# Performance work log

Hardware: AMD Instinct MI355X
Metric: run time of the kernel (lower is better)

The kernel has to match this reference:

```python
import jax, jax.numpy as jnp
import numpy as np

B, DIN, DOUT, DC, K, DB = 4096, 512, 512, 64, 16, 256
NEG = 0.01
LN_EPS = 1e-5

def _lrelu(v):
    return jnp.where(v >= 0, v, NEG * v)

def setup_inputs() -> dict:
    key = jax.random.key(0)
    ks = jax.random.split(key, 12)
    bound = 1.0 / np.sqrt(DIN)
    def u(k, shape, b):
        return jax.random.uniform(k, shape, jnp.float32, -b, b)
    return {
        "x": jax.random.normal(ks[0], (B, DIN), jnp.float32),
        "c": jax.random.normal(ks[1], (B, DC), jnp.float32),
        "ln_gamma": jnp.ones((DIN,), jnp.float32),
        "ln_beta": jnp.zeros((DIN,), jnp.float32),
        "w1": u(ks[2], (DC, DB), 1.0 / np.sqrt(DC)),
        "b1": u(ks[3], (DB,), 1.0 / np.sqrt(DC)),
        "wr": u(ks[4], (DB, DB), 1.0 / np.sqrt(DB)),
        "br": u(ks[5], (DB,), 1.0 / np.sqrt(DB)),
        "w2": u(ks[6], (DB, K), 1.0 / np.sqrt(DB)),
        "b2": u(ks[7], (K,), 1.0 / np.sqrt(DB)),
        "W": u(ks[8], (K, DIN, DOUT), bound),
        "bvec": u(ks[9], (K, DOUT), bound),
    }

def reference(x, c, ln_gamma, ln_beta, w1, b1, wr, br, w2, b2, W, bvec):
    # DenseActivation: LayerNorm + LeakyReLU (dropout_rate=0)
    mu = jnp.mean(x, axis=-1, keepdims=True)
    var = jnp.mean(jnp.square(x - mu), axis=-1, keepdims=True)
    xn = (x - mu) * jax.lax.rsqrt(var + LN_EPS) * ln_gamma + ln_beta
    a = _lrelu(xn)  # [B, DIN]
    # basis_functions(c): Linear -> 1 preactivation resnet block -> LeakyReLU -> Linear
    h = c @ w1 + b1                      # [B, DB]
    h = h + (_lrelu(h) @ wr + br)        # residual block (preactivation)
    h = _lrelu(h)                        # activate_output
    bf = h @ w2 + b2                     # [B, K]
    # out_b = x_b^T (sum_k bf_bk W_k) + bf_b @ bias ; reordered contraction
    xw = jnp.einsum("bi,kio->bko", a, W)       # [B, K, DOUT]
    out = jnp.einsum("bk,bko->bo", bf, xw)     # [B, DOUT]
    out = out + bf @ bvec
    return out
```

## Files before the change

### kernel.cpp

```cpp
#include <hip/hip_runtime.h>


#define LRELU(v) ((v) >= 0.f ? (v) : 0.01f * (v))

typedef _Float16 f16x8 __attribute__((ext_vector_type(8)));
typedef float f32x4 __attribute__((ext_vector_type(4)));

#define GL16(gp, lp) __builtin_amdgcn_global_load_lds(                      \
    (const __attribute__((address_space(1))) void*)(gp),                    \
    (__attribute__((address_space(3))) void*)(lp), 16, 0, 0)

#define MFMA16(a, b, c) __builtin_amdgcn_mfma_f32_16x16x32_f16((a), (b), (c), 0, 0, 0)

__global__ __launch_bounds__(256) void prep_kernel(
    const float* __restrict__ x, const float* __restrict__ gam,
    const float* __restrict__ bet, _Float16* __restrict__ a,
    const float* __restrict__ c, const float* __restrict__ w1,
    const float* __restrict__ b1, const float* __restrict__ wr,
    const float* __restrict__ br, const float* __restrict__ w2,
    const float* __restrict__ b2, float* __restrict__ bfo,
    const float* __restrict__ W, _Float16* __restrict__ Wt)
{
    __shared__ __align__(16) char smem[18432];
    int tid = threadIdx.x;
    int blk = blockIdx.x;

    if (blk < 512) {
        float* c_l  = (float*)smem;
        float* lr_l = (float*)(smem + 2048);
        float* h_l  = (float*)(smem + 10240);
        int b0 = blk * 8;

        for (int i = tid; i < 8 * 64; i += 256) c_l[i] = c[(size_t)b0 * 64 + i];

        float w1c[64];
#pragma unroll
        for (int u = 0; u < 64; ++u) w1c[u] = w1[u * 256 + tid];
        float b1s = b1[tid];
        __syncthreads();

        float h1[8];
#pragma unroll
        for (int r = 0; r < 8; ++r) h1[r] = b1s;
#pragma unroll
        for (int j4 = 0; j4 < 16; ++j4) {
#pragma unroll
            for (int r = 0; r < 8; ++r) {
                float4 cv = *(const float4*)&c_l[r * 64 + j4 * 4];
                h1[r] += cv.x * w1c[j4 * 4 + 0] + cv.y * w1c[j4 * 4 + 1] +
                         cv.z * w1c[j4 * 4 + 2] + cv.w * w1c[j4 * 4 + 3];
            }
        }
#pragma unroll
        for (int r = 0; r < 8; ++r) lr_l[r * 256 + tid] = LRELU(h1[r]);
        __syncthreads();

        float brv = br[tid];
        float h2[8];
#pragma unroll
        for (int r = 0; r < 8; ++r) h2[r] = h1[r] + brv;

#pragma unroll 1
        for (int jc = 0; jc < 8; ++jc) {
            float w8[32];
#pragma unroll
            for (int u = 0; u < 32; ++u) w8[u] = wr[(jc * 32 + u) * 256 + tid];
#pragma unroll
            for (int j4 = 0; j4 < 8; ++j4) {
#pragma unroll
                for (int r = 0; r < 8; ++r) {
                    float4 lv = *(const float4*)&lr_l[r * 256 + jc * 32 + j4 * 4];
                    h2[r] += lv.x * w8[j4 * 4 + 0] + lv.y * w8[j4 * 4 + 1] +
                             lv.z * w8[j4 * 4 + 2] + lv.w * w8[j4 * 4 + 3];
                }
            }
        }
#pragma unroll
        for (int r = 0; r < 8; ++r) h_l[r * 256 + tid] = LRELU(h2[r]);
        __syncthreads();

        if (tid < 128) {
            int r = tid >> 4, k = tid & 15;
            float s = b2[k];
#pragma unroll 1
            for (int qc = 0; qc < 8; ++qc) {
                float wv[32];
#pragma unroll
                for (int u = 0; u < 32; ++u) wv[u] = w2[(qc * 32 + u) * 16 + k];
#pragma unroll
                for (int q4 = 0; q4 < 8; ++q4) {
                    float4 hv = *(const float4*)&h_l[r * 256 + qc * 32 + q4 * 4];
                    s += hv.x * wv[q4 * 4 + 0] + hv.y * wv[q4 * 4 + 1] +
                         hv.z * wv[q4 * 4 + 2] + hv.w * wv[q4 * 4 + 3];
                }
            }
            bfo[(size_t)(b0 + r) * 16 + k] = s;
        }

    } else if (blk < 1536) {
        float* t = (float*)smem;
        int bid = blk - 512;
        int k  = bid >> 6;
        int it = (bid >> 3) & 7;
        int ot = bid & 7;
        int i0 = it * 64, o0 = ot * 64;

        int rr = tid >> 4, c4 = (tid & 15) * 4;
#pragma unroll
        for (int p = 0; p < 4; ++p) {
            int r = p * 16 + rr;
            float4 v = *(const float4*)&W[((size_t)(k * 512 + i0 + r)) * 512 + o0 + c4];
            t[r * 65 + c4 + 0] = v.x;
            t[r * 65 + c4 + 1] = v.y;
            t[r * 65 + c4 + 2] = v.z;
            t[r * 65 + c4 + 3] = v.w;
        }
        __syncthreads();

        int ol = tid >> 2, c0 = (tid & 3) * 16;
        _Float16 hb[16] __attribute__((aligned(16)));
#pragma unroll
        for (int u = 0; u < 16; ++u) hb[u] = (_Float16)t[(c0 + u) * 65 + ol];
        _Float16* dst = &Wt[(size_t)(o0 + ol) * 8192 + k * 512 + i0 + c0];
        *(float4*)dst       = *(const float4*)&hb[0];
        *(float4*)(dst + 8) = *(const float4*)&hb[8];

    } else {
        int lane = tid & 63;
        int row  = (blk - 1536) * 4 + (tid >> 6);
        const float* xr = x + (size_t)row * 512 + lane * 8;
        float4 v0 = *(const float4*)xr;
        float4 v1 = *(const float4*)(xr + 4);

        float s = v0.x + v0.y + v0.z + v0.w + v1.x + v1.y + v1.z + v1.w;
#pragma unroll
        for (int m = 1; m < 64; m <<= 1) s += __shfl_xor(s, m);
        float mean = s * (1.f / 512.f);

        float d, s2 = 0.f;
        d = v0.x - mean; s2 += d * d;
        d = v0.y - mean; s2 += d * d;
        d = v0.z - mean; s2 += d * d;
        d = v0.w - mean; s2 += d * d;
        d = v1.x - mean; s2 += d * d;
        d = v1.y - mean; s2 += d * d;
        d = v1.z - mean; s2 += d * d;
        d = v1.w - mean; s2 += d * d;
#pragma unroll
        for (int m = 1; m < 64; m <<= 1) s2 += __shfl_xor(s2, m);
        float rstd = rsqrtf(s2 * (1.f / 512.f) + 1e-5f);

        float4 g0 = *(const float4*)&gam[lane * 8];
        float4 g1 = *(const float4*)&gam[lane * 8 + 4];
        float4 b0 = *(const float4*)&bet[lane * 8];
        float4 b1v = *(const float4*)&bet[lane * 8 + 4];

        _Float16 o8[8] __attribute__((aligned(16)));
        float y;
        y = (v0.x - mean) * rstd * g0.x + b0.x;  y = LRELU(y); o8[0] = (_Float16)y;
        y = (v0.y - mean) * rstd * g0.y + b0.y;  y = LRELU(y); o8[1] = (_Float16)y;
        y = (v0.z - mean) * rstd * g0.z + b0.z;  y = LRELU(y); o8[2] = (_Float16)y;
        y = (v0.w - mean) * rstd * g0.w + b0.w;  y = LRELU(y); o8[3] = (_Float16)y;
        y = (v1.x - mean) * rstd * g1.x + b1v.x; y = LRELU(y); o8[4] = (_Float16)y;
        y = (v1.y - mean) * rstd * g1.y + b1v.y; y = LRELU(y); o8[5] = (_Float16)y;
        y = (v1.z - mean) * rstd * g1.z + b1v.z; y = LRELU(y); o8[6] = (_Float16)y;
        y = (v1.w - mean) * rstd * g1.w + b1v.w; y = LRELU(y); o8[7] = (_Float16)y;

        *(float4*)&a[(size_t)row * 512 + lane * 8] = *(const float4*)o8;
    }
}

template <int NSPLIT>
__global__ __launch_bounds__(256, 2) void gemm_kernel(
    const _Float16* __restrict__ A,
    const _Float16* __restrict__ Wt,
    const float* __restrict__ bfg,
    const float* __restrict__ bvec,
    _Float16* __restrict__ pout)
{
    constexpr int KTN = 16 / NSPLIT;
    constexpr int NT  = KTN * 8;

    __shared__ _Float16 As[2][128 * 64];
    __shared__ _Float16 Bs[2][128 * 64];

    const int tid = threadIdx.x;
    const int bid = blockIdx.x;
    const int split = bid % NSPLIT;
    const int mn  = bid / NSPLIT;
    const int n0  = (mn & 3) * 128;
    const int bm0 = (mn >> 2) * 128;
    const int kt0 = split * KTN;

    const int lane = tid & 63, wid = tid >> 6;
    const int wm = wid >> 1, wn = wid & 1;
    const int l16 = lane & 15, lg = lane >> 4;

    _Float16 s16[KTN][4];
#pragma unroll
    for (int kt = 0; kt < KTN; ++kt)
#pragma unroll
        for (int f = 0; f < 4; ++f)
            s16[kt][f] = (_Float16)
                bfg[(size_t)(bm0 + wm * 64 + f * 16 + l16) * 16 + kt0 + kt];

    const int brow = tid >> 3;
    const int swc  = (tid & 7) ^ (brow & 7);
    const _Float16* aAs = A  + (size_t)(bm0 + brow) * 512  + swc * 8;
    const _Float16* aBs = Wt + (size_t)(n0  + brow) * 8192 + swc * 8;

    auto STAGE = [&](int t, int buf) {
        const int ka = (t & 7) * 64;
        const size_t kb = (size_t)(kt0 + (t >> 3)) * 512 + ka;
        char* la = (char*)&As[buf][0] + tid * 16;
        char* lb = (char*)&Bs[buf][0] + tid * 16;
#pragma unroll
        for (int p = 0; p < 4; ++p) {
            GL16(aAs + (size_t)(p * 32) * 512 + ka, la + p * 4096);
            GL16(aBs + (size_t)(p * 32) * 8192 + kb, lb + p * 4096);
        }
    };

    const int swr = l16 & 7;
    const int aRowByte = (wm * 64 + l16) * 128;
    const int bRowByte = (wn * 64 + l16) * 128;
    const int sw0 = ((0 + lg) ^ swr) << 4;
    const int sw1 = ((4 + lg) ^ swr) << 4;

    const f32x4 z4 = {0.f, 0.f, 0.f, 0.f};
    f32x4 acc[4][4];
#pragma unroll
    for (int f = 0; f < 4; ++f)
#pragma unroll
        for (int nf = 0; nf < 4; ++nf) acc[f][nf] = z4;

    STAGE(0, 0);
    STAGE(1, 1);
    asm volatile("s_waitcnt vmcnt(8)" ::: "memory");
    __builtin_amdgcn_s_barrier();
    __builtin_amdgcn_sched_barrier(0);

#pragma unroll
    for (int kt = 0; kt < KTN; ++kt) {
#pragma unroll 1
        for (int t2 = 0; t2 < 8; ++t2) {
            const int t = kt * 8 + t2;
            const int cur = t & 1;
            const char* Ab = (const char*)&As[cur][0];
            const char* Bb = (const char*)&Bs[cur][0];
            const int tt = t + 2;
            const bool st = (tt < NT);
            char* sAd = (char*)&As[cur][0] + tid * 16;
            char* sBd = (char*)&Bs[cur][0] + tid * 16;
            const int ka = (tt & 7) * 64;
            const size_t kb = (size_t)(kt0 + (tt >> 3)) * 512 + ka;

            f16x8 bA0 = *(const f16x8*)(Bb + bRowByte + 0 * 2048 + sw0);
            f16x8 bA1 = *(const f16x8*)(Bb + bRowByte + 0 * 2048 + sw1);
            f16x8 bB0 = *(const f16x8*)(Bb + bRowByte + 1 * 2048 + sw0);
            f16x8 bB1 = *(const f16x8*)(Bb + bRowByte + 1 * 2048 + sw1);
            f16x8 bC0 = *(const f16x8*)(Bb + bRowByte + 2 * 2048 + sw0);
            f16x8 bC1 = *(const f16x8*)(Bb + bRowByte + 2 * 2048 + sw1);
            f16x8 bD0 = *(const f16x8*)(Bb + bRowByte + 3 * 2048 + sw0);
            f16x8 bD1 = *(const f16x8*)(Bb + bRowByte + 3 * 2048 + sw1);
            f16x8 a00 = *(const f16x8*)(Ab + aRowByte + 0 * 2048 + sw0);
            f16x8 a01 = *(const f16x8*)(Ab + aRowByte + 0 * 2048 + sw1);
            f16x8 a10 = *(const f16x8*)(Ab + aRowByte + 1 * 2048 + sw0);
            f16x8 a11 = *(const f16x8*)(Ab + aRowByte + 1 * 2048 + sw1);
            __builtin_amdgcn_s_barrier();

            {
                const _Float16 s0 = s16[kt][0], s1 = s16[kt][1];
                a00 *= s0; a01 *= s0; a10 *= s1; a11 *= s1;
                __builtin_amdgcn_s_setprio(1);
                acc[0][0] = MFMA16(a00, bA0, acc[0][0]);
                acc[0][0] = MFMA16(a01, bA1, acc[0][0]);
                acc[0][1] = MFMA16(a00, bB0, acc[0][1]);
                acc[0][1] = MFMA16(a01, bB1, acc[0][1]);
                acc[0][2] = MFMA16(a00, bC0, acc[0][2]);
                acc[0][2] = MFMA16(a01, bC1, acc[0][2]);
                acc[0][3] = MFMA16(a00, bD0, acc[0][3]);
                acc[0][3] = MFMA16(a01, bD1, acc[0][3]);
                acc[1][0] = MFMA16(a10, bA0, acc[1][0]);
                acc[1][0] = MFMA16(a11, bA1, acc[1][0]);
                acc[1][1] = MFMA16(a10, bB0, acc[1][1]);
                acc[1][1] = MFMA16(a11, bB1, acc[1][1]);
                acc[1][2] = MFMA16(a10, bC0, acc[1][2]);
                acc[1][2] = MFMA16(a11, bC1, acc[1][2]);
                acc[1][3] = MFMA16(a10, bD0, acc[1][3]);
                acc[1][3] = MFMA16(a11, bD1, acc[1][3]);
                __builtin_amdgcn_s_setprio(0);
            }
            __builtin_amdgcn_s_barrier();

            f16x8 a20 = *(const f16x8*)(Ab + aRowByte + 2 * 2048 + sw0);
            f16x8 a21 = *(const f16x8*)(Ab + aRowByte + 2 * 2048 + sw1);
            f16x8 a30 = *(const f16x8*)(Ab + aRowByte + 3 * 2048 + sw0);
            f16x8 a31 = *(const f16x8*)(Ab + aRowByte + 3 * 2048 + sw1);
            if (st) {
                GL16(aBs + (size_t)(0 * 32) * 8192 + kb, sBd + 0 * 4096);
                GL16(aBs + (size_t)(1 * 32) * 8192 + kb, sBd + 1 * 4096);
                GL16(aBs + (size_t)(2 * 32) * 8192 + kb, sBd + 2 * 4096);
                GL16(aBs + (size_t)(3 * 32) * 8192 + kb, sBd + 3 * 4096);
                GL16(aAs + (size_t)(0 * 32) * 512 + ka, sAd + 0 * 4096);
                GL16(aAs + (size_t)(2 * 32) * 512 + ka, sAd + 2 * 4096);
            }
            __builtin_amdgcn_s_barrier();

            {
                const _Float16 s2 = s16[kt][2], s3 = s16[kt][3];
                a20 *= s2; a21 *= s2; a30 *= s3; a31 *= s3;
                __builtin_amdgcn_s_setprio(1);
                acc[2][0] = MFMA16(a20, bA0, acc[2][0]);
                acc[2][0] = MFMA16(a21, bA1, acc[2][0]);
                acc[2][1] = MFMA16(a20, bB0, acc[2][1]);
                acc[2][1] = MFMA16(a21, bB1, acc[2][1]);
                acc[2][2] = MFMA16(a20, bC0, acc[2][2]);
                acc[2][2] = MFMA16(a21, bC1, acc[2][2]);
                acc[2][3] = MFMA16(a20, bD0, acc[2][3]);
                acc[2][3] = MFMA16(a21, bD1, acc[2][3]);
                acc[3][0] = MFMA16(a30, bA0, acc[3][0]);
                acc[3][0] = MFMA16(a31, bA1, acc[3][0]);
                acc[3][1] = MFMA16(a30, bB0, acc[3][1]);
                acc[3][1] = MFMA16(a31, bB1, acc[3][1]);
                acc[3][2] = MFMA16(a30, bC0, acc[3][2]);
                acc[3][2] = MFMA16(a31, bC1, acc[3][2]);
                acc[3][3] = MFMA16(a30, bD0, acc[3][3]);
                acc[3][3] = MFMA16(a31, bD1, acc[3][3]);
                __builtin_amdgcn_s_setprio(0);
            }
            __builtin_amdgcn_s_barrier();

            if (st) {
                GL16(aAs + (size_t)(1 * 32) * 512 + ka, sAd + 1 * 4096);
                GL16(aAs + (size_t)(3 * 32) * 512 + ka, sAd + 3 * 4096);
                asm volatile("s_waitcnt vmcnt(8)" ::: "memory");
            } else {
                asm volatile("s_waitcnt vmcnt(0)" ::: "memory");
            }
            __builtin_amdgcn_s_barrier();
            __builtin_amdgcn_sched_barrier(0);
        }
    }

    _Float16* op = pout + (size_t)split * (4096 * 512);
    const int colBase = n0 + wn * 64 + l16;
    float bvv[KTN][4];
#pragma unroll
    for (int kt = 0; kt < KTN; ++kt)
#pragma unroll
        for (int nf = 0; nf < 4; ++nf)
            bvv[kt][nf] = bvec[(kt0 + kt) * 512 + colBase + nf * 16];

#pragma unroll
    for (int f = 0; f < 4; ++f)
#pragma unroll
        for (int j = 0; j < 4; ++j) {
            const int grow = bm0 + wm * 64 + f * 16 + lg * 4 + j;
            const float* bfr = &bfg[(size_t)grow * 16 + kt0];
            float bfl[KTN];
#pragma unroll
            for (int kt = 0; kt < KTN; ++kt) bfl[kt] = bfr[kt];
            _Float16* orow = op + (size_t)grow * 512 + colBase;
#pragma unroll
            for (int nf = 0; nf < 4; ++nf) {
                float v = acc[f][nf][j];
#pragma unroll
                for (int kt = 0; kt < KTN; ++kt) v += bfl[kt] * bvv[kt][nf];
                orow[nf * 16] = (_Float16)v;
            }
        }
}

__global__ __launch_bounds__(256) void reduce_kernel(const _Float16* __restrict__ p,
                                                     float* __restrict__ out,
                                                     int nsplit)
{
    size_t i   = (size_t)blockIdx.x * 256 + threadIdx.x;
    size_t off = i * 8;
    float s[8] = {0.f, 0.f, 0.f, 0.f, 0.f, 0.f, 0.f, 0.f};
    for (int sp = 0; sp < nsplit; ++sp) {
        f16x8 v = *(const f16x8*)&p[(size_t)sp * 2097152 + off];
#pragma unroll
        for (int u = 0; u < 8; ++u) s[u] += (float)v[u];
    }
    float4 o0 = {s[0], s[1], s[2], s[3]};
    float4 o1 = {s[4], s[5], s[6], s[7]};
    *(float4*)&out[off]     = o0;
    *(float4*)&out[off + 4] = o1;
}

extern "C" void kernel_launch(void* const* d_in, const int* in_sizes, int n_in,
                              void* d_out, int out_size, void* d_ws, size_t ws_size,
                              hipStream_t stream)
{
    const float* x    = (const float*)d_in[0];
    const float* c    = (const float*)d_in[1];
    const float* gam  = (const float*)d_in[2];
    const float* bet  = (const float*)d_in[3];
    const float* w1   = (const float*)d_in[4];
    const float* b1   = (const float*)d_in[5];
    const float* wr   = (const float*)d_in[6];
    const float* br   = (const float*)d_in[7];
    const float* w2   = (const float*)d_in[8];
    const float* b2   = (const float*)d_in[9];
    const float* W    = (const float*)d_in[10];
    const float* bvec = (const float*)d_in[11];
    float* out = (float*)d_out;

    const int nsplit = 4;
    const size_t partBytes = (size_t)nsplit * 4096 * 512 * sizeof(_Float16);

    char* ws = (char*)d_ws;
    _Float16* part = (_Float16*)ws;
    _Float16* Wt   = (_Float16*)(ws + partBytes);
    _Float16* af   = (_Float16*)(ws + partBytes + (8u << 20));
    float*    bf   = (float*)(ws + partBytes + (12u << 20));

    prep_kernel<<<dim3(2560), dim3(256), 0, stream>>>(
        x, gam, bet, af, c, w1, b1, wr, br, w2, b2, bf, W, Wt);

    gemm_kernel<4><<<dim3(512), dim3(256), 0, stream>>>(af, Wt, bf, bvec, part);

    reduce_kernel<<<dim3(1024), dim3(256), 0, stream>>>(part, out, nsplit);
}
```

Before: 82.89 us.

## Replace double-buffered GEMM pipeline with single-buffer, more splits and higher occupancy

```diff
diff --git a/kernel.cpp b/kernel.cpp
--- a/kernel.cpp
+++ b/kernel.cpp
@@ -171,7 +171,7 @@
 }
 
 template <int NSPLIT>
-__global__ __launch_bounds__(256, 2) void gemm_kernel(
+__global__ __launch_bounds__(256, 4) void gemm_kernel(
     const _Float16* __restrict__ A,
     const _Float16* __restrict__ Wt,
     const float* __restrict__ bfg,
@@ -179,10 +179,9 @@
     _Float16* __restrict__ pout)
 {
     constexpr int KTN = 16 / NSPLIT;
-    constexpr int NT  = KTN * 8;
-
-    __shared__ _Float16 As[2][128 * 64];
-    __shared__ _Float16 Bs[2][128 * 64];
+
+    __shared__ _Float16 As[128 * 64];
+    __shared__ _Float16 Bs[128 * 64];
 
     const int tid = threadIdx.x;
     const int bid = blockIdx.x;
@@ -204,22 +203,12 @@
             s16[kt][f] = (_Float16)
                 bfg[(size_t)(bm0 + wm * 64 + f * 16 + l16) * 16 + kt0 + kt];
 
-    const int brow = tid >> 3;
-    const int swc  = (tid & 7) ^ (brow & 7);
-    const _Float16* aAs = A  + (size_t)(bm0 + brow) * 512  + swc * 8;
-    const _Float16* aBs = Wt + (size_t)(n0  + brow) * 8192 + swc * 8;
-
-    auto STAGE = [&](int t, int buf) {
-        const int ka = (t & 7) * 64;
-        const size_t kb = (size_t)(kt0 + (t >> 3)) * 512 + ka;
-        char* la = (char*)&As[buf][0] + tid * 16;
-        char* lb = (char*)&Bs[buf][0] + tid * 16;
-#pragma unroll
-        for (int p = 0; p < 4; ++p) {
-            GL16(aAs + (size_t)(p * 32) * 512 + ka, la + p * 4096);
-            GL16(aBs + (size_t)(p * 32) * 8192 + kb, lb + p * 4096);
-        }
-    };
+    const int srow = tid >> 3;
+    const int swc  = (tid & 7) ^ (srow & 7);
+    const _Float16* aAs = A  + (size_t)(bm0 + srow) * 512  + swc * 8;
+    const _Float16* aBs = Wt + (size_t)(n0  + srow) * 8192 + swc * 8;
+    char* lA = (char*)As + tid * 16;
+    char* lB = (char*)Bs + tid * 16;
 
     const int swr = l16 & 7;
     const int aRowByte = (wm * 64 + l16) * 128;
@@ -234,26 +223,24 @@
 #pragma unroll
         for (int nf = 0; nf < 4; ++nf) acc[f][nf] = z4;
 
-    STAGE(0, 0);
-    STAGE(1, 1);
-    asm volatile("s_waitcnt vmcnt(8)" ::: "memory");
-    __builtin_amdgcn_s_barrier();
-    __builtin_amdgcn_sched_barrier(0);
+    const char* Ab = (const char*)As;
+    const char* Bb = (const char*)Bs;
 
 #pragma unroll
     for (int kt = 0; kt < KTN; ++kt) {
+        const size_t kcol = (size_t)(kt0 + kt) * 512;
+        const _Float16 s0 = s16[kt][0], s1 = s16[kt][1];
+        const _Float16 s2 = s16[kt][2], s3 = s16[kt][3];
 #pragma unroll 1
-        for (int t2 = 0; t2 < 8; ++t2) {
-            const int t = kt * 8 + t2;
-            const int cur = t & 1;
-            const char* Ab = (const char*)&As[cur][0];
-            const char* Bb = (const char*)&Bs[cur][0];
-            const int tt = t + 2;
-            const bool st = (tt < NT);
-            char* sAd = (char*)&As[cur][0] + tid * 16;
-            char* sBd = (char*)&Bs[cur][0] + tid * 16;
-            const int ka = (tt & 7) * 64;
-            const size_t kb = (size_t)(kt0 + (tt >> 3)) * 512 + ka;
+        for (int ks = 0; ks < 8; ++ks) {
+            const int ka = ks * 64;
+            const size_t kb = kcol + ka;
+#pragma unroll
+            for (int p = 0; p < 4; ++p) {
+                GL16(aAs + (size_t)(p * 32) * 512 + ka, lA + p * 4096);
+                GL16(aBs + (size_t)(p * 32) * 8192 + kb, lB + p * 4096);
+            }
+            __syncthreads();
 
             f16x8 bA0 = *(const f16x8*)(Bb + bRowByte + 0 * 2048 + sw0);
             f16x8 bA1 = *(const f16x8*)(Bb + bRowByte + 0 * 2048 + sw1);
@@ -263,14 +250,12 @@
             f16x8 bC1 = *(const f16x8*)(Bb + bRowByte + 2 * 2048 + sw1);
             f16x8 bD0 = *(const f16x8*)(Bb + bRowByte + 3 * 2048 + sw0);
             f16x8 bD1 = *(const f16x8*)(Bb + bRowByte + 3 * 2048 + sw1);
-            f16x8 a00 = *(const f16x8*)(Ab + aRowByte + 0 * 2048 + sw0);
-            f16x8 a01 = *(const f16x8*)(Ab + aRowByte + 0 * 2048 + sw1);
-            f16x8 a10 = *(const f16x8*)(Ab + aRowByte + 1 * 2048 + sw0);
-            f16x8 a11 = *(const f16x8*)(Ab + aRowByte + 1 * 2048 + sw1);
-            __builtin_amdgcn_s_barrier();
 
             {
-                const _Float16 s0 = s16[kt][0], s1 = s16[kt][1];
+                f16x8 a00 = *(const f16x8*)(Ab + aRowByte + 0 * 2048 + sw0);
+                f16x8 a01 = *(const f16x8*)(Ab + aRowByte + 0 * 2048 + sw1);
+                f16x8 a10 = *(const f16x8*)(Ab + aRowByte + 1 * 2048 + sw0);
+                f16x8 a11 = *(const f16x8*)(Ab + aRowByte + 1 * 2048 + sw1);
                 a00 *= s0; a01 *= s0; a10 *= s1; a11 *= s1;
                 __builtin_amdgcn_s_setprio(1);
                 acc[0][0] = MFMA16(a00, bA0, acc[0][0]);
@@ -291,24 +276,11 @@
                 acc[1][3] = MFMA16(a11, bD1, acc[1][3]);
                 __builtin_amdgcn_s_setprio(0);
             }
-            __builtin_amdgcn_s_barrier();
-
-            f16x8 a20 = *(const f16x8*)(Ab + aRowByte + 2 * 2048 + sw0);
-            f16x8 a21 = *(const f16x8*)(Ab + aRowByte + 2 * 2048 + sw1);
-            f16x8 a30 = *(const f16x8*)(Ab + aRowByte + 3 * 2048 + sw0);
-            f16x8 a31 = *(const f16x8*)(Ab + aRowByte + 3 * 2048 + sw1);
-            if (st) {
-                GL16(aBs + (size_t)(0 * 32) * 8192 + kb, sBd + 0 * 4096);
-                GL16(aBs + (size_t)(1 * 32) * 8192 + kb, sBd + 1 * 4096);
-                GL16(aBs + (size_t)(2 * 32) * 8192 + kb, sBd + 2 * 4096);
-                GL16(aBs + (size_t)(3 * 32) * 8192 + kb, sBd + 3 * 4096);
-                GL16(aAs + (size_t)(0 * 32) * 512 + ka, sAd + 0 * 4096);
-                GL16(aAs + (size_t)(2 * 32) * 512 + ka, sAd + 2 * 4096);
-            }
-            __builtin_amdgcn_s_barrier();
-
             {
-                const _Float16 s2 = s16[kt][2], s3 = s16[kt][3];
+                f16x8 a20 = *(const f16x8*)(Ab + aRowByte + 2 * 2048 + sw0);
+                f16x8 a21 = *(const f16x8*)(Ab + aRowByte + 2 * 2048 + sw1);
+                f16x8 a30 = *(const f16x8*)(Ab + aRowByte + 3 * 2048 + sw0);
+                f16x8 a31 = *(const f16x8*)(Ab + aRowByte + 3 * 2048 + sw1);
                 a20 *= s2; a21 *= s2; a30 *= s3; a31 *= s3;
                 __builtin_amdgcn_s_setprio(1);
                 acc[2][0] = MFMA16(a20, bA0, acc[2][0]);
@@ -329,17 +301,7 @@
                 acc[3][3] = MFMA16(a31, bD1, acc[3][3]);
                 __builtin_amdgcn_s_setprio(0);
             }
-            __builtin_amdgcn_s_barrier();
-
-            if (st) {
-                GL16(aAs + (size_t)(1 * 32) * 512 + ka, sAd + 1 * 4096);
-                GL16(aAs + (size_t)(3 * 32) * 512 + ka, sAd + 3 * 4096);
-                asm volatile("s_waitcnt vmcnt(8)" ::: "memory");
-            } else {
-                asm volatile("s_waitcnt vmcnt(0)" ::: "memory");
-            }
-            __builtin_amdgcn_s_barrier();
-            __builtin_amdgcn_sched_barrier(0);
+            __syncthreads();
         }
     }
 
@@ -408,7 +370,7 @@
     const float* bvec = (const float*)d_in[11];
     float* out = (float*)d_out;
 
-    const int nsplit = 4;
+    const int nsplit = 8;
     const size_t partBytes = (size_t)nsplit * 4096 * 512 * sizeof(_Float16);
 
     char* ws = (char*)d_ws;
@@ -420,7 +382,7 @@
     prep_kernel<<<dim3(2560), dim3(256), 0, stream>>>(
         x, gam, bet, af, c, w1, b1, wr, br, w2, b2, bf, W, Wt);
 
-    gemm_kernel<4><<<dim3(512), dim3(256), 0, stream>>>(af, Wt, bf, bvec, part);
+    gemm_kernel<8><<<dim3(1024), dim3(256), 0, stream>>>(af, Wt, bf, bvec, part);
 
     reduce_kernel<<<dim3(1024), dim3(256), 0, stream>>>(part, out, nsplit);
 }
```

Result: slower. 196.6 us (+137.2%).

## Reorder contraction to GEMM over DIN with in-register k reduction, drop split-K

Applied to the files above, without the earlier changes.

```diff
diff --git a/kernel.cpp b/kernel.cpp
--- a/kernel.cpp
+++ b/kernel.cpp
@@ -19,7 +19,7 @@
     const float* __restrict__ b1, const float* __restrict__ wr,
     const float* __restrict__ br, const float* __restrict__ w2,
     const float* __restrict__ b2, float* __restrict__ bfo,
-    const float* __restrict__ W, _Float16* __restrict__ Wt)
+    const float* __restrict__ W, _Float16* __restrict__ Wp)
 {
     __shared__ __align__(16) char smem[18432];
     int tid = threadIdx.x;
@@ -121,7 +121,7 @@
         _Float16 hb[16] __attribute__((aligned(16)));
 #pragma unroll
         for (int u = 0; u < 16; ++u) hb[u] = (_Float16)t[(c0 + u) * 65 + ol];
-        _Float16* dst = &Wt[(size_t)(o0 + ol) * 8192 + k * 512 + i0 + c0];
+        _Float16* dst = &Wp[((size_t)(o0 + ol) * 16 + k) * 512 + i0 + c0];
         *(float4*)dst       = *(const float4*)&hb[0];
         *(float4*)(dst + 8) = *(const float4*)&hb[8];
 
@@ -170,54 +170,40 @@
     }
 }
 
-template <int NSPLIT>
 __global__ __launch_bounds__(256, 2) void gemm_kernel(
     const _Float16* __restrict__ A,
-    const _Float16* __restrict__ Wt,
+    const _Float16* __restrict__ Wp,
     const float* __restrict__ bfg,
     const float* __restrict__ bvec,
-    _Float16* __restrict__ pout)
+    float* __restrict__ out)
 {
-    constexpr int KTN = 16 / NSPLIT;
-    constexpr int NT  = KTN * 8;
+    constexpr int NT = 8;
 
     __shared__ _Float16 As[2][128 * 64];
     __shared__ _Float16 Bs[2][128 * 64];
 
     const int tid = threadIdx.x;
     const int bid = blockIdx.x;
-    const int split = bid % NSPLIT;
-    const int mn  = bid / NSPLIT;
-    const int n0  = (mn & 3) * 128;
-    const int bm0 = (mn >> 2) * 128;
-    const int kt0 = split * KTN;
+    const int bm0 = (bid >> 6) * 128;
+    const int g0  = (bid & 63) * 128;
 
     const int lane = tid & 63, wid = tid >> 6;
     const int wm = wid >> 1, wn = wid & 1;
     const int l16 = lane & 15, lg = lane >> 4;
 
-    _Float16 s16[KTN][4];
-#pragma unroll
-    for (int kt = 0; kt < KTN; ++kt)
-#pragma unroll
-        for (int f = 0; f < 4; ++f)
-            s16[kt][f] = (_Float16)
-                bfg[(size_t)(bm0 + wm * 64 + f * 16 + l16) * 16 + kt0 + kt];
-
     const int brow = tid >> 3;
     const int swc  = (tid & 7) ^ (brow & 7);
-    const _Float16* aAs = A  + (size_t)(bm0 + brow) * 512  + swc * 8;
-    const _Float16* aBs = Wt + (size_t)(n0  + brow) * 8192 + swc * 8;
+    const _Float16* aAs = A  + (size_t)(bm0 + brow) * 512 + swc * 8;
+    const _Float16* aBs = Wp + (size_t)(g0  + brow) * 512 + swc * 8;
 
     auto STAGE = [&](int t, int buf) {
-        const int ka = (t & 7) * 64;
-        const size_t kb = (size_t)(kt0 + (t >> 3)) * 512 + ka;
+        const int ka = t * 64;
         char* la = (char*)&As[buf][0] + tid * 16;
         char* lb = (char*)&Bs[buf][0] + tid * 16;
 #pragma unroll
         for (int p = 0; p < 4; ++p) {
             GL16(aAs + (size_t)(p * 32) * 512 + ka, la + p * 4096);
-            GL16(aBs + (size_t)(p * 32) * 8192 + kb, lb + p * 4096);
+            GL16(aBs + (size_t)(p * 32) * 512 + ka, lb + p * 4096);
         }
     };
 
@@ -240,154 +226,118 @@
     __builtin_amdgcn_s_barrier();
     __builtin_amdgcn_sched_barrier(0);
 
-#pragma unroll
-    for (int kt = 0; kt < KTN; ++kt) {
 #pragma unroll 1
-        for (int t2 = 0; t2 < 8; ++t2) {
-            const int t = kt * 8 + t2;
-            const int cur = t & 1;
-            const char* Ab = (const char*)&As[cur][0];
-            const char* Bb = (const char*)&Bs[cur][0];
-            const int tt = t + 2;
-            const bool st = (tt < NT);
-            char* sAd = (char*)&As[cur][0] + tid * 16;
-            char* sBd = (char*)&Bs[cur][0] + tid * 16;
-            const int ka = (tt & 7) * 64;
-            const size_t kb = (size_t)(kt0 + (tt >> 3)) * 512 + ka;
-
-            f16x8 bA0 = *(const f16x8*)(Bb + bRowByte + 0 * 2048 + sw0);
-            f16x8 bA1 = *(const f16x8*)(Bb + bRowByte + 0 * 2048 + sw1);
-            f16x8 bB0 = *(const f16x8*)(Bb + bRowByte + 1 * 2048 + sw0);
-            f16x8 bB1 = *(const f16x8*)(Bb + bRowByte + 1 * 2048 + sw1);
-            f16x8 bC0 = *(const f16x8*)(Bb + bRowByte + 2 * 2048 + sw0);
-            f16x8 bC1 = *(const f16x8*)(Bb + bRowByte + 2 * 2048 + sw1);
-            f16x8 bD0 = *(const f16x8*)(Bb + bRowByte + 3 * 2048 + sw0);
-            f16x8 bD1 = *(const f16x8*)(Bb + bRowByte + 3 * 2048 + sw1);
-            f16x8 a00 = *(const f16x8*)(Ab + aRowByte + 0 * 2048 + sw0);
-            f16x8 a01 = *(const f16x8*)(Ab + aRowByte + 0 * 2048 + sw1);
-            f16x8 a10 = *(const f16x8*)(Ab + aRowByte + 1 * 2048 + sw0);
-            f16x8 a11 = *(const f16x8*)(Ab + aRowByte + 1 * 2048 + sw1);
-            __builtin_amdgcn_s_barrier();
-
-            {
-                const _Float16 s0 = s16[kt][0], s1 = s16[kt][1];
-                a00 *= s0; a01 *= s0; a10 *= s1; a11 *= s1;
-                __builtin_amdgcn_s_setprio(1);
-                acc[0][0] = MFMA16(a00, bA0, acc[0][0]);
-                acc[0][0] = MFMA16(a01, bA1, acc[0][0]);
-                acc[0][1] = MFMA16(a00, bB0, acc[0][1]);
-                acc[0][1] = MFMA16(a01, bB1, acc[0][1]);
-                acc[0][2] = MFMA16(a00, bC0, acc[0][2]);
-                acc[0][2] = MFMA16(a01, bC1, acc[0][2]);
-                acc[0][3] = MFMA16(a00, bD0, acc[0][3]);
-                acc[0][3] = MFMA16(a01, bD1, acc[0][3]);
-                acc[1][0] = MFMA16(a10, bA0, acc[1][0]);
-                acc[1][0] = MFMA16(a11, bA1, acc[1][0]);
-                acc[1][1] = MFMA16(a10, bB0, acc[1][1]);
-                acc[1][1] = MFMA16(a11, bB1, acc[1][1]);
-                acc[1][2] = MFMA16(a10, bC0, acc[1][2]);
-                acc[1][2] = MFMA16(a11, bC1, acc[1][2]);
-                acc[1][3] = MFMA16(a10, bD0, acc[1][3]);
-                acc[1][3] = MFMA16(a11, bD1, acc[1][3]);
-                __builtin_amdgcn_s_setprio(0);
+    for (int t = 0; t < NT; ++t) {
+        const int cur = t & 1;
+        const char* Ab = (const char*)&As[cur][0];
+        const char* Bb = (const char*)&Bs[cur][0];
+        const bool st = (t + 2 < NT);
+        char* sAd = (char*)&As[cur][0] + tid * 16;
+        char* sBd = (char*)&Bs[cur][0] + tid * 16;
+        const int ka = (t + 2) * 64;
+
+        f16x8 bA0 = *(const f16x8*)(Bb + bRowByte + 0 * 2048 + sw0);
+        f16x8 bA1 = *(const f16x8*)(Bb + bRowByte + 0 * 2048 + sw1);
+        f16x8 bB0 = *(const f16x8*)(Bb + bRowByte + 1 * 2048 + sw0);
+        f16x8 bB1 = *(const f16x8*)(Bb + bRowByte + 1 * 2048 + sw1);
+        f16x8 bC0 = *(const f16x8*)(Bb + bRowByte + 2 * 2048 + sw0);
+        f16x8 bC1 = *(const f16x8*)(Bb + bRowByte + 2 * 2048 + sw1);
+        f16x8 bD0 = *(const f16x8*)(Bb + bRowByte + 3 * 2048 + sw0);
+        f16x8 bD1 = *(const f16x8*)(Bb + bRowByte + 3 * 2048 + sw1);
+        f16x8 a00 = *(const f16x8*)(Ab + aRowByte + 0 * 2048 + sw0);
+        f16x8 a01 = *(const f16x8*)(Ab + aRowByte + 0 * 2048 + sw1);
+        f16x8 a10 = *(const f16x8*)(Ab + aRowByte + 1 * 2048 + sw0);
+        f16x8 a11 = *(const f16x8*)(Ab + aRowByte + 1 * 2048 + sw1);
+        __builtin_amdgcn_s_barrier();
+
+        __builtin_amdgcn_s_setprio(1);
+        acc[0][0] = MFMA16(a00, bA0, acc[0][0]);
+        acc[0][0] = MFMA16(a01, bA1, acc[0][0]);
+        acc[0][1] = MFMA16(a00, bB0, acc[0][1]);
+        acc[0][1] = MFMA16(a01, bB1, acc[0][1]);
+        acc[0][2] = MFMA16(a00, bC0, acc[0][2]);
+        acc[0][2] = MFMA16(a01, bC1, acc[0][2]);
+        acc[0][3] = MFMA16(a00, bD0, acc[0][3]);
+        acc[0][3] = MFMA16(a01, bD1, acc[0][3]);
+        acc[1][0] = MFMA16(a10, bA0, acc[1][0]);
+        acc[1][0] = MFMA16(a11, bA1, acc[1][0]);
+        acc[1][1] = MFMA16(a10, bB0, acc[1][1]);
+        acc[1][1] = MFMA16(a11, bB1, acc[1][1]);
+        acc[1][2] = MFMA16(a10, bC0, acc[1][2]);
+        acc[1][2] = MFMA16(a11, bC1, acc[1][2]);
+        acc[1][3] = MFMA16(a10, bD0, acc[1][3]);
+        acc[1][3] = MFMA16(a11, bD1, acc[1][3]);
+        __builtin_amdgcn_s_setprio(0);
+        __builtin_amdgcn_s_barrier();
+
+        f16x8 a20 = *(const f16x8*)(Ab + aRowByte + 2 * 2048 + sw0);
+        f16x8 a21 = *(const f16x8*)(Ab + aRowByte + 2 * 2048 + sw1);
+        f16x8 a30 = *(const f16x8*)(Ab + aRowByte + 3 * 2048 + sw0);
+        f16x8 a31 = *(const f16x8*)(Ab + aRowByte + 3 * 2048 + sw1);
+        if (st) {
+            GL16(aBs + (size_t)(0 * 32) * 512 + ka, sBd + 0 * 4096);
+            GL16(aBs + (size_t)(1 * 32) * 512 + ka, sBd + 1 * 4096);
+            GL16(aBs + (size_t)(2 * 32) * 512 + ka, sBd + 2 * 4096);
+            GL16(aBs + (size_t)(3 * 32) * 512 + ka, sBd + 3 * 4096);
+            GL16(aAs + (size_t)(0 * 32) * 512 + ka, sAd + 0 * 4096);
+            GL16(aAs + (size_t)(2 * 32) * 512 + ka, sAd + 2 * 4096);
+        }
+        __builtin_amdgcn_s_barrier();
+
+        __builtin_amdgcn_s_setprio(1);
+        acc[2][0] = MFMA16(a20, bA0, acc[2][0]);
+        acc[2][0] = MFMA16(a21, bA1, acc[2][0]);
+        acc[2][1] = MFMA16(a20, bB0, acc[2][1]);
+        acc[2][1] = MFMA16(a21, bB1, acc[2][1]);
+        acc[2][2] = MFMA16(a20, bC0, acc[2][2]);
+        acc[2][2] = MFMA16(a21, bC1, acc[2][2]);
+        acc[2][3] = MFMA16(a20, bD0, acc[2][3]);
+        acc[2][3] = MFMA16(a21, bD1, acc[2][3]);
+        acc[3][0] = MFMA16(a30, bA0, acc[3][0]);
+        acc[3][0] = MFMA16(a31, bA1, acc[3][0]);
+        acc[3][1] = MFMA16(a30, bB0, acc[3][1]);
+        acc[3][1] = MFMA16(a31, bB1, acc[3][1]);
+        acc[3][2] = MFMA16(a30, bC0, acc[3][2]);
+        acc[3][2] = MFMA16(a31, bC1, acc[3][2]);
+        acc[3][3] = MFMA16(a30, bD0, acc[3][3]);
+        acc[3][3] = MFMA16(a31, bD1, acc[3][3]);
+        __builtin_amdgcn_s_setprio(0);
+        __builtin_amdgcn_s_barrier();
+
+        if (st) {
+            GL16(aAs + (size_t)(1 * 32) * 512 + ka, sAd + 1 * 4096);
+            GL16(aAs + (size_t)(3 * 32) * 512 + ka, sAd + 3 * 4096);
+            asm volatile("s_waitcnt vmcnt(8)" ::: "memory");
+        } else {
+            asm volatile("s_waitcnt vmcnt(0)" ::: "memory");
+        }
+        __builtin_amdgcn_s_barrier();
+        __builtin_amdgcn_sched_barrier(0);
+    }
+
+    const int oBase = (g0 >> 4) + wn * 4;
+    float bvl[4];
+#pragma unroll
+    for (int nf = 0; nf < 4; ++nf)
+        bvl[nf] = bvec[(size_t)l16 * 512 + oBase + nf];
+
+#pragma unroll
+    for (int f = 0; f < 4; ++f)
+#pragma unroll
+        for (int j = 0; j < 4; ++j) {
+            const int row = bm0 + wm * 64 + f * 16 + lg * 4 + j;
+            const float bfl = bfg[(size_t)row * 16 + l16];
+#pragma unroll
+            for (int nf = 0; nf < 4; ++nf) {
+                float t = (acc[f][nf][j] + bvl[nf]) * bfl;
+                t += __shfl_xor(t, 1);
+                t += __shfl_xor(t, 2);
+                t += __shfl_xor(t, 4);
+                t += __shfl_xor(t, 8);
+                if (l16 == 0)
+                    out[(size_t)row * 512 + oBase + nf] = t;
             }
-            __builtin_amdgcn_s_barrier();
-
-            f16x8 a20 = *(const f16x8*)(Ab + aRowByte + 2 * 2048 + sw0);
-            f16x8 a21 = *(const f16x8*)(Ab + aRowByte + 2 * 2048 + sw1);
-            f16x8 a30 = *(const f16x8*)(Ab + aRowByte + 3 * 2048 + sw0);
-            f16x8 a31 = *(const f16x8*)(Ab + aRowByte + 3 * 2048 + sw1);
-            if (st) {
-                GL16(aBs + (size_t)(0 * 32) * 8192 + kb, sBd + 0 * 4096);
-                GL16(aBs + (size_t)(1 * 32) * 8192 + kb, sBd + 1 * 4096);
-                GL16(aBs + (size_t)(2 * 32) * 8192 + kb, sBd + 2 * 4096);
-                GL16(aBs + (size_t)(3 * 32) * 8192 + kb, sBd + 3 * 4096);
-                GL16(aAs + (size_t)(0 * 32) * 512 + ka, sAd + 0 * 4096);
-                GL16(aAs + (size_t)(2 * 32) * 512 + ka, sAd + 2 * 4096);
-            }
-            __builtin_amdgcn_s_barrier();
-
-            {
-                const _Float16 s2 = s16[kt][2], s3 = s16[kt][3];
-                a20 *= s2; a21 *= s2; a30 *= s3; a31 *= s3;
-                __builtin_amdgcn_s_setprio(1);
-                acc[2][0] = MFMA16(a20, bA0, acc[2][0]);
-                acc[2][0] = MFMA16(a21, bA1, acc[2][0]);
-                acc[2][1] = MFMA16(a20, bB0, acc[2][1]);
-                acc[2][1] = MFMA16(a21, bB1, acc[2][1]);
-                acc[2][2] = MFMA16(a20, bC0, acc[2][2]);
-                acc[2][2] = MFMA16(a21, bC1, acc[2][2]);
-                acc[2][3] = MFMA16(a20, bD0, acc[2][3]);
-                acc[2][3] = MFMA16(a21, bD1, acc[2][3]);
-                acc[3][0] = MFMA16(a30, bA0, acc[3][0]);
-                acc[3][0] = MFMA16(a31, bA1, acc[3][0]);
-                acc[3][1] = MFMA16(a30, bB0, acc[3][1]);
-                acc[3][1] = MFMA16(a31, bB1, acc[3][1]);
-                acc[3][2] = MFMA16(a30, bC0, acc[3][2]);
-                acc[3][2] = MFMA16(a31, bC1, acc[3][2]);
-                acc[3][3] = MFMA16(a30, bD0, acc[3][3]);
-                acc[3][3] = MFMA16(a31, bD1, acc[3][3]);
-                __builtin_amdgcn_s_setprio(0);
-            }
-            __builtin_amdgcn_s_barrier();
-
-            if (st) {
-                GL16(aAs + (size_t)(1 * 32) * 512 + ka, sAd + 1 * 4096);
-                GL16(aAs + (size_t)(3 * 32) * 512 + ka, sAd + 3 * 4096);
-                asm volatile("s_waitcnt vmcnt(8)" ::: "memory");
-            } else {
-                asm volatile("s_waitcnt vmcnt(0)" ::: "memory");
-            }
-            __builtin_amdgcn_s_barrier();
-            __builtin_amdgcn_sched_barrier(0);
-        }
-    }
-
-    _Float16* op = pout + (size_t)split * (4096 * 512);
-    const int colBase = n0 + wn * 64 + l16;
-    float bvv[KTN][4];
-#pragma unroll
-    for (int kt = 0; kt < KTN; ++kt)
-#pragma unroll
-        for (int nf = 0; nf < 4; ++nf)
-            bvv[kt][nf] = bvec[(kt0 + kt) * 512 + colBase + nf * 16];
-
-#pragma unroll
-    for (int f = 0; f < 4; ++f)
-#pragma unroll
-        for (int j = 0; j < 4; ++j) {
-            const int grow = bm0 + wm * 64 + f * 16 + lg * 4 + j;
-            const float* bfr = &bfg[(size_t)grow * 16 + kt0];
-            float bfl[KTN];
-#pragma unroll
-            for (int kt = 0; kt < KTN; ++kt) bfl[kt] = bfr[kt];
-            _Float16* orow = op + (size_t)grow * 512 + colBase;
-#pragma unroll
-            for (int nf = 0; nf < 4; ++nf) {
-                float v = acc[f][nf][j];
-#pragma unroll
-                for (int kt = 0; kt < KTN; ++kt) v += bfl[kt] * bvv[kt][nf];
-                orow[nf * 16] = (_Float16)v;
-            }
-        }
-}
-
-__global__ __launch_bounds__(256) void reduce_kernel(const _Float16* __restrict__ p,
-                                                     float* __restrict__ out,
-                                                     int nsplit)
-{
-    size_t i   = (size_t)blockIdx.x * 256 + threadIdx.x;
-    size_t off = i * 8;
-    float s[8] = {0.f, 0.f, 0.f, 0.f, 0.f, 0.f, 0.f, 0.f};
-    for (int sp = 0; sp < nsplit; ++sp) {
-        f16x8 v = *(const f16x8*)&p[(size_t)sp * 2097152 + off];
-#pragma unroll
-        for (int u = 0; u < 8; ++u) s[u] += (float)v[u];
-    }
-    float4 o0 = {s[0], s[1], s[2], s[3]};
-    float4 o1 = {s[4], s[5], s[6], s[7]};
-    *(float4*)&out[off]     = o0;
-    *(float4*)&out[off + 4] = o1;
+        }
 }
 
 extern "C" void kernel_launch(void* const* d_in, const int* in_sizes, int n_in,
@@ -408,19 +358,13 @@
     const float* bvec = (const float*)d_in[11];
     float* out = (float*)d_out;
 
-    const int nsplit = 4;
-    const size_t partBytes = (size_t)nsplit * 4096 * 512 * sizeof(_Float16);
-
     char* ws = (char*)d_ws;
-    _Float16* part = (_Float16*)ws;
-    _Float16* Wt   = (_Float16*)(ws + partBytes);
-    _Float16* af   = (_Float16*)(ws + partBytes + (8u << 20));
-    float*    bf   = (float*)(ws + partBytes + (12u << 20));
+    _Float16* Wp = (_Float16*)ws;
+    _Float16* af = (_Float16*)(ws + (8u << 20));
+    float*    bf = (float*)(ws + (12u << 20));
 
     prep_kernel<<<dim3(2560), dim3(256), 0, stream>>>(
-        x, gam, bet, af, c, w1, b1, wr, br, w2, b2, bf, W, Wt);
-
-    gemm_kernel<4><<<dim3(512), dim3(256), 0, stream>>>(af, Wt, bf, bvec, part);
-
-    reduce_kernel<<<dim3(1024), dim3(256), 0, stream>>>(part, out, nsplit);
+        x, gam, bet, af, c, w1, b1, wr, br, w2, b2, bf, W, Wp);
+
+    gemm_kernel<<<dim3(2048), dim3(256), 0, stream>>>(af, Wp, bf, bvec, out);
 }
```

After: 115.7 us. +39.6%, slower.
